# Kernel optimization log

Hardware: AMD Instinct MI355X
Metric: run time of the kernel (lower is better)

Reference implementation:

```python
import jax, jax.numpy as jnp
import numpy as np

N = 131072  # number of attention rows (batch * queries)
M = 100     # number of 2D Gaussian basis functions (10x10 grid in original repo)
TWO_PI = 6.283185307179586


def inv2x2(A):
    """Closed-form inverse and determinant of batched 2x2 matrices."""
    a = A[..., 0, 0]; b = A[..., 0, 1]; c = A[..., 1, 0]; d = A[..., 1, 1]
    det = a * d - b * c
    row0 = jnp.stack([d, -b], axis=-1)
    row1 = jnp.stack([-c, a], axis=-1)
    inv = jnp.stack([row0, row1], axis=-2) / det[..., None, None]
    return inv, det


def setup_inputs() -> dict:
    key = jax.random.key(0)
    k1, k2, k3, k4 = jax.random.split(key, 4)
    # linear canonical parameter eta = Sigma^{-1} mu
    eta = 0.5 * jax.random.normal(k1, (N, 2), dtype=jnp.float32)
    # SPD precision P so that theta[:,2:6] = -0.5 * P (valid exp-family params)
    L = 0.3 * jax.random.normal(k2, (N, 2, 2), dtype=jnp.float32)
    P = L @ jnp.swapaxes(L, -1, -2) + 0.5 * jnp.eye(2, dtype=jnp.float32)
    theta = jnp.concatenate([eta, (-0.5 * P).reshape(N, 4)], axis=1)  # [N,6]
    # Gaussian basis functions: means in [0,1]^2, small diagonal covariances
    basis_mu = jax.random.uniform(k3, (M, 2), dtype=jnp.float32)
    var = jax.random.uniform(k4, (M, 2), dtype=jnp.float32, minval=0.01, maxval=0.05)
    basis_sigma = jax.vmap(jnp.diag)(var)  # [M,2,2]
    return {"theta": theta, "basis_mu": basis_mu, "basis_sigma": basis_sigma}


def reference(theta, basis_mu, basis_sigma):
    # Sigma = symmetrized inverse of (-2 * quadratic canonical params)
    P = -2.0 * theta[:, 2:6].reshape(-1, 2, 2)          # [N,2,2]
    Pinv, _ = inv2x2(P)
    Sigma = 0.5 * (Pinv + jnp.swapaxes(Pinv, -1, -2))   # [N,2,2]
    Mu = jnp.einsum('nij,nj->ni', Sigma, theta[:, 0:2])  # [N,2]
    # r[n,j] = integral N(t; Mu_n, Sigma_n) N(t; mu_j, S_j) dt
    #        = N(Mu_n - mu_j; 0, Sigma_n + S_j)
    C = Sigma[:, None, :, :] + basis_sigma[None, :, :, :]  # [N,M,2,2]
    diff = Mu[:, None, :] - basis_mu[None, :, :]           # [N,M,2]
    Cinv, detC = inv2x2(C)
    quad = jnp.einsum('nmi,nmij,nmj->nm', diff, Cinv, diff)
    r = jnp.exp(-0.5 * quad) / (TWO_PI * jnp.sqrt(detC))   # [N,M]
    return r
```

## Files before the change

kernel.cpp:

```cpp
#include <hip/hip_runtime.h>

#define M_BASIS 100
constexpr float INV_TWO_PI = 0.15915494309189535f;

__global__ __launch_bounds__(256) void cs_kernel(
    const float* __restrict__ theta,
    const float* __restrict__ basis_mu,
    const float* __restrict__ basis_sigma,
    float* __restrict__ out,
    int N)
{
    const int lane = threadIdx.x & 63;
    const int waves_per_block = blockDim.x >> 6;
    const int wave_id = blockIdx.x * waves_per_block + (threadIdx.x >> 6);
    const int num_waves = gridDim.x * waves_per_block;

    const bool active = (lane < (M_BASIS / 2));

    float4 mu2 = make_float4(0.f, 0.f, 0.f, 0.f);
    float4 sA  = make_float4(1.f, 0.f, 0.f, 1.f);
    float4 sB  = make_float4(1.f, 0.f, 0.f, 1.f);
    if (active) {
        mu2 = ((const float4*)basis_mu)[lane];
        sA  = ((const float4*)basis_sigma)[2 * lane];
        sB  = ((const float4*)basis_sigma)[2 * lane + 1];
    }

    #pragma unroll 2
    for (int n = wave_id; n < N; n += num_waves) {
        const float* th = theta + n * 6;
        float2 e  = *(const float2*)(th);
        float2 qa = *(const float2*)(th + 2);
        float2 qb = *(const float2*)(th + 4);

        float detQ = qa.x * qb.y - qa.y * qb.x;
        float r    = __builtin_amdgcn_rcpf(detQ);
        float h    = -0.5f * r;
        float S00  = qb.y * h;
        float S11  = qa.x * h;
        float S01  = (qa.y + qb.x) * (-0.5f * h);
        float Mu0  = S00 * e.x + S01 * e.y;
        float Mu1  = S01 * e.x + S11 * e.y;

        if (active) {
            float c00 = S00 + sA.x, c01 = S01 + sA.y;
            float c10 = S01 + sA.z, c11 = S11 + sA.w;
            float d0 = Mu0 - mu2.x, d1 = Mu1 - mu2.y;
            float detC = c00 * c11 - c01 * c10;
            float rs   = __builtin_amdgcn_rsqf(detC);
            float invC = rs * rs;
            float t = d0 * d0, u = d1 * d1, dd = d0 * d1;
            float num = t * c11 + u * c00 - dd * (c01 + c10);
            float r0 = __expf(-0.5f * num * invC) * (INV_TWO_PI * rs);

            float e00 = S00 + sB.x, e01 = S01 + sB.y;
            float e10 = S01 + sB.z, e11 = S11 + sB.w;
            float f0 = Mu0 - mu2.z, f1 = Mu1 - mu2.w;
            float detE = e00 * e11 - e01 * e10;
            float rsE  = __builtin_amdgcn_rsqf(detE);
            float invE = rsE * rsE;
            float tE = f0 * f0, uE = f1 * f1, ddE = f0 * f1;
            float numE = tE * e11 + uE * e00 - ddE * (e01 + e10);
            float r1 = __expf(-0.5f * numE * invE) * (INV_TWO_PI * rsE);

            ((float2*)(out + (size_t)n * M_BASIS))[lane] = make_float2(r0, r1);
        }
    }
}

extern "C" void kernel_launch(void* const* d_in, const int* in_sizes, int n_in,
                              void* d_out, int out_size, void* d_ws, size_t ws_size,
                              hipStream_t stream) {
    const float* theta      = (const float*)d_in[0];
    const float* basis_mu   = (const float*)d_in[1];
    const float* basis_sig  = (const float*)d_in[2];
    float* out = (float*)d_out;

    int N = in_sizes[0] / 6;
    int block = 256;
    int grid = 4096;
    hipLaunchKernelGGL(cs_kernel, dim3(grid), dim3(block), 0, stream,
                       theta, basis_mu, basis_sig, out, N);
}
```

Measured before the change: 88.30 us.

## Stage output rows in shared memory and write contiguous float4 block stores

Each block now handles a fixed group of 32 rows: every wave computes 8 rows into a shared-memory tile, and after a barrier the whole block writes the tile to global memory with contiguous float4 stores. The grid switches from a grid-stride loop to one block per 32 rows. This targets the partially active waves (only 50 of 64 lanes store 8-byte values) in the output-bandwidth-bound store path. In exchange it adds LDS traffic, a __syncthreads, and far more blocks to launch.

```diff
diff --git a/kernel.cpp b/kernel.cpp
--- a/kernel.cpp
+++ b/kernel.cpp
@@ -1,6 +1,8 @@
 #include <hip/hip_runtime.h>
 
 #define M_BASIS 100
+#define ROWS_PER_BLOCK 32
+#define ROWS_PER_WAVE 8
 constexpr float INV_TWO_PI = 0.15915494309189535f;
 
 __global__ __launch_bounds__(256) void cs_kernel(
@@ -10,11 +12,11 @@
     float* __restrict__ out,
     int N)
 {
-    const int lane = threadIdx.x & 63;
-    const int waves_per_block = blockDim.x >> 6;
-    const int wave_id = blockIdx.x * waves_per_block + (threadIdx.x >> 6);
-    const int num_waves = gridDim.x * waves_per_block;
+    __shared__ float tile[ROWS_PER_BLOCK * M_BASIS];
 
+    const int tid  = threadIdx.x;
+    const int lane = tid & 63;
+    const int wave = tid >> 6;
     const bool active = (lane < (M_BASIS / 2));
 
     float4 mu2 = make_float4(0.f, 0.f, 0.f, 0.f);
@@ -26,45 +28,59 @@
         sB  = ((const float4*)basis_sigma)[2 * lane + 1];
     }
 
-    #pragma unroll 2
-    for (int n = wave_id; n < N; n += num_waves) {
-        const float* th = theta + n * 6;
-        float2 e  = *(const float2*)(th);
-        float2 qa = *(const float2*)(th + 2);
-        float2 qb = *(const float2*)(th + 4);
+    const int row0 = blockIdx.x * ROWS_PER_BLOCK + wave * ROWS_PER_WAVE;
 
-        float detQ = qa.x * qb.y - qa.y * qb.x;
-        float r    = __builtin_amdgcn_rcpf(detQ);
-        float h    = -0.5f * r;
-        float S00  = qb.y * h;
-        float S11  = qa.x * h;
-        float S01  = (qa.y + qb.x) * (-0.5f * h);
-        float Mu0  = S00 * e.x + S01 * e.y;
-        float Mu1  = S01 * e.x + S11 * e.y;
+    #pragma unroll
+    for (int k = 0; k < ROWS_PER_WAVE; ++k) {
+        const int n = row0 + k;
+        if (n < N) {
+            const float* th = theta + n * 6;
+            float2 e  = *(const float2*)(th);
+            float2 qa = *(const float2*)(th + 2);
+            float2 qb = *(const float2*)(th + 4);
 
-        if (active) {
-            float c00 = S00 + sA.x, c01 = S01 + sA.y;
-            float c10 = S01 + sA.z, c11 = S11 + sA.w;
-            float d0 = Mu0 - mu2.x, d1 = Mu1 - mu2.y;
-            float detC = c00 * c11 - c01 * c10;
-            float rs   = __builtin_amdgcn_rsqf(detC);
-            float invC = rs * rs;
-            float t = d0 * d0, u = d1 * d1, dd = d0 * d1;
-            float num = t * c11 + u * c00 - dd * (c01 + c10);
-            float r0 = __expf(-0.5f * num * invC) * (INV_TWO_PI * rs);
+            float detQ = qa.x * qb.y - qa.y * qb.x;
+            float r    = __builtin_amdgcn_rcpf(detQ);
+            float h    = -0.5f * r;
+            float S00  = qb.y * h;
+            float S11  = qa.x * h;
+            float S01  = (qa.y + qb.x) * (-0.5f * h);
+            float Mu0  = S00 * e.x + S01 * e.y;
+            float Mu1  = S01 * e.x + S11 * e.y;
 
-            float e00 = S00 + sB.x, e01 = S01 + sB.y;
-            float e10 = S01 + sB.z, e11 = S11 + sB.w;
-            float f0 = Mu0 - mu2.z, f1 = Mu1 - mu2.w;
-            float detE = e00 * e11 - e01 * e10;
-            float rsE  = __builtin_amdgcn_rsqf(detE);
-            float invE = rsE * rsE;
-            float tE = f0 * f0, uE = f1 * f1, ddE = f0 * f1;
-            float numE = tE * e11 + uE * e00 - ddE * (e01 + e10);
-            float r1 = __expf(-0.5f * numE * invE) * (INV_TWO_PI * rsE);
+            if (active) {
+                float c00 = S00 + sA.x, c01 = S01 + sA.y;
+                float c10 = S01 + sA.z, c11 = S11 + sA.w;
+                float d0 = Mu0 - mu2.x, d1 = Mu1 - mu2.y;
+                float detC = c00 * c11 - c01 * c10;
+                float rs   = __builtin_amdgcn_rsqf(detC);
+                float invC = rs * rs;
+                float num = d0 * d0 * c11 + d1 * d1 * c00 - d0 * d1 * (c01 + c10);
+                float r0 = __expf(-0.5f * num * invC) * (INV_TWO_PI * rs);
 
-            ((float2*)(out + (size_t)n * M_BASIS))[lane] = make_float2(r0, r1);
+                float e00 = S00 + sB.x, e01 = S01 + sB.y;
+                float e10 = S01 + sB.z, e11 = S11 + sB.w;
+                float f0 = Mu0 - mu2.z, f1 = Mu1 - mu2.w;
+                float detE = e00 * e11 - e01 * e10;
+                float rsE  = __builtin_amdgcn_rsqf(detE);
+                float invE = rsE * rsE;
+                float numE = f0 * f0 * e11 + f1 * f1 * e00 - f0 * f1 * (e01 + e10);
+                float r1 = __expf(-0.5f * numE * invE) * (INV_TWO_PI * rsE);
+
+                ((float2*)(tile + (wave * ROWS_PER_WAVE + k) * M_BASIS))[lane] =
+                    make_float2(r0, r1);
+            }
         }
+    }
+
+    __syncthreads();
+
+    const int rows_valid = min(ROWS_PER_BLOCK, N - blockIdx.x * ROWS_PER_BLOCK);
+    const int valid4 = rows_valid * (M_BASIS / 4);
+    float4* obase = (float4*)(out + (size_t)blockIdx.x * ROWS_PER_BLOCK * M_BASIS);
+    const float4* t4 = (const float4*)tile;
+    for (int k = tid; k < valid4; k += 256) {
+        obase[k] = t4[k];
     }
 }
 
@@ -78,7 +94,7 @@
 
     int N = in_sizes[0] / 6;
     int block = 256;
-    int grid = 4096;
+    int grid = (N + ROWS_PER_BLOCK - 1) / ROWS_PER_BLOCK;
     hipLaunchKernelGGL(cs_kernel, dim3(grid), dim3(block), 0, stream,
                        theta, basis_mu, basis_sig, out, N);
 }
```

Measured after the change: 88.65 us. Within noise of the previous version (+0.4%).

## Split into per-row precompute kernel and flat one-output-per-thread kernel

Applied to the files above, without the earlier changes.

Moves the per-row 2x2 inversion and mean computation into a separate kernel that writes 8 floats per row to workspace. The main kernel then uses a flat grid with one output element per thread, reading basis parameters from shared memory. The flat layout gives fully coalesced output stores, where the old wave-per-row loop left 14 of 64 lanes idle. The cost is an extra launch, a workspace round trip of about 4 MB, and redundant row loads and integer division by 100 in every thread.

```diff
diff --git a/kernel.cpp b/kernel.cpp
--- a/kernel.cpp
+++ b/kernel.cpp
@@ -3,69 +3,77 @@
 #define M_BASIS 100
 constexpr float INV_TWO_PI = 0.15915494309189535f;
 
+__global__ __launch_bounds__(256) void row_kernel(
+    const float* __restrict__ theta, float* __restrict__ rp, int N)
+{
+    int n = blockIdx.x * 256 + threadIdx.x;
+    if (n >= N) return;
+    const float* th = theta + n * 6;
+    float2 e  = *(const float2*)(th);
+    float2 qa = *(const float2*)(th + 2);
+    float2 qb = *(const float2*)(th + 4);
+
+    float detQ = qa.x * qb.y - qa.y * qb.x;
+    float r    = __builtin_amdgcn_rcpf(detQ);
+    float h    = -0.5f * r;
+    float S00  = qb.y * h;
+    float S11  = qa.x * h;
+    float S01  = (qa.y + qb.x) * (-0.5f * h);
+    float Mu0  = S00 * e.x + S01 * e.y;
+    float Mu1  = S01 * e.x + S11 * e.y;
+
+    float4* o = (float4*)(rp + 8 * (size_t)n);
+    o[0] = make_float4(S00, S01, S11, Mu0);
+    o[1] = make_float4(Mu1, 2.0f * S01, 0.0f, 0.0f);
+}
+
 __global__ __launch_bounds__(256) void cs_kernel(
-    const float* __restrict__ theta,
+    const float* __restrict__ rp,
     const float* __restrict__ basis_mu,
     const float* __restrict__ basis_sigma,
     float* __restrict__ out,
-    int N)
+    int total)
 {
-    const int lane = threadIdx.x & 63;
-    const int waves_per_block = blockDim.x >> 6;
-    const int wave_id = blockIdx.x * waves_per_block + (threadIdx.x >> 6);
-    const int num_waves = gridDim.x * waves_per_block;
+    __shared__ float B00[M_BASIS], B11[M_BASIS], Bs[M_BASIS], Bp[M_BASIS];
+    __shared__ float M0[M_BASIS], M1[M_BASIS];
 
-    const bool active = (lane < (M_BASIS / 2));
+    int t = threadIdx.x;
+    if (t < M_BASIS) {
+        float4 s = ((const float4*)basis_sigma)[t];
+        float2 m = ((const float2*)basis_mu)[t];
+        B00[t] = s.x; B11[t] = s.w;
+        Bs[t]  = s.y + s.z;
+        Bp[t]  = s.y * s.z;
+        M0[t]  = m.x; M1[t]  = m.y;
+    }
+    __syncthreads();
 
-    float4 mu2 = make_float4(0.f, 0.f, 0.f, 0.f);
-    float4 sA  = make_float4(1.f, 0.f, 0.f, 1.f);
-    float4 sB  = make_float4(1.f, 0.f, 0.f, 1.f);
-    if (active) {
-        mu2 = ((const float4*)basis_mu)[lane];
-        sA  = ((const float4*)basis_sigma)[2 * lane];
-        sB  = ((const float4*)basis_sigma)[2 * lane + 1];
-    }
+    int i = blockIdx.x * 256 + t;
+    if (i >= total) return;
+    unsigned n = (unsigned)i / 100u;
+    unsigned j = (unsigned)i - n * 100u;
 
-    #pragma unroll 2
-    for (int n = wave_id; n < N; n += num_waves) {
-        const float* th = theta + n * 6;
-        float2 e  = *(const float2*)(th);
-        float2 qa = *(const float2*)(th + 2);
-        float2 qb = *(const float2*)(th + 4);
+    const float4* r4 = (const float4*)(rp + 8 * (size_t)n);
+    float4 ra = r4[0];
+    float4 rb = r4[1];
+    float S00 = ra.x, S01 = ra.y, S11 = ra.z, Mu0 = ra.w;
+    float Mu1 = rb.x, twoS01 = rb.y;
 
-        float detQ = qa.x * qb.y - qa.y * qb.x;
-        float r    = __builtin_amdgcn_rcpf(detQ);
-        float h    = -0.5f * r;
-        float S00  = qb.y * h;
-        float S11  = qa.x * h;
-        float S01  = (qa.y + qb.x) * (-0.5f * h);
-        float Mu0  = S00 * e.x + S01 * e.y;
-        float Mu1  = S01 * e.x + S11 * e.y;
+    float c00 = S00 + B00[j];
+    float c11 = S11 + B11[j];
+    float tq  = fmaf(S01, Bs[j], fmaf(S01, S01, Bp[j]));
+    float detC = fmaf(c00, c11, -tq);
 
-        if (active) {
-            float c00 = S00 + sA.x, c01 = S01 + sA.y;
-            float c10 = S01 + sA.z, c11 = S11 + sA.w;
-            float d0 = Mu0 - mu2.x, d1 = Mu1 - mu2.y;
-            float detC = c00 * c11 - c01 * c10;
-            float rs   = __builtin_amdgcn_rsqf(detC);
-            float invC = rs * rs;
-            float t = d0 * d0, u = d1 * d1, dd = d0 * d1;
-            float num = t * c11 + u * c00 - dd * (c01 + c10);
-            float r0 = __expf(-0.5f * num * invC) * (INV_TWO_PI * rs);
+    float d0 = Mu0 - M0[j];
+    float d1 = Mu1 - M1[j];
+    float cs = twoS01 + Bs[j];
+    float num = d0 * d0 * c11;
+    num = fmaf(d1 * d1, c00, num);
+    num = fmaf(-(d0 * d1), cs, num);
 
-            float e00 = S00 + sB.x, e01 = S01 + sB.y;
-            float e10 = S01 + sB.z, e11 = S11 + sB.w;
-            float f0 = Mu0 - mu2.z, f1 = Mu1 - mu2.w;
-            float detE = e00 * e11 - e01 * e10;
-            float rsE  = __builtin_amdgcn_rsqf(detE);
-            float invE = rsE * rsE;
-            float tE = f0 * f0, uE = f1 * f1, ddE = f0 * f1;
-            float numE = tE * e11 + uE * e00 - ddE * (e01 + e10);
-            float r1 = __expf(-0.5f * numE * invE) * (INV_TWO_PI * rsE);
-
-            ((float2*)(out + (size_t)n * M_BASIS))[lane] = make_float2(r0, r1);
-        }
-    }
+    float rs = __builtin_amdgcn_rsqf(detC);
+    float ex = __expf(-0.5f * num * (rs * rs));
+    out[i] = ex * (INV_TWO_PI * rs);
 }
 
 extern "C" void kernel_launch(void* const* d_in, const int* in_sizes, int n_in,
@@ -75,10 +83,16 @@
     const float* basis_mu   = (const float*)d_in[1];
     const float* basis_sig  = (const float*)d_in[2];
     float* out = (float*)d_out;
+    float* rp  = (float*)d_ws;
 
     int N = in_sizes[0] / 6;
-    int block = 256;
-    int grid = 4096;
-    hipLaunchKernelGGL(cs_kernel, dim3(grid), dim3(block), 0, stream,
-                       theta, basis_mu, basis_sig, out, N);
+    int total = out_size;
+
+    int gridA = (N + 255) / 256;
+    hipLaunchKernelGGL(row_kernel, dim3(gridA), dim3(256), 0, stream,
+                       theta, rp, N);
+
+    int gridB = (total + 255) / 256;
+    hipLaunchKernelGGL(cs_kernel, dim3(gridB), dim3(256), 0, stream,
+                       rp, basis_mu, basis_sig, out, total);
 }
```

Result: slower. 103.9 us (+17.7%).

## Process two rows per wave with float4 nontemporal stores of four basis outputs

Applied to the files above, without the earlier changes.

Each wave now handles a pair of rows. Lanes 0-24 compute the first row and lanes 25-49 the second, with four basis functions per lane written as one 16-byte nontemporal store. Basis parameters are pre-reduced into sums and products so fewer ops are needed per element, and the grid is halved to match. The goal is wider, contiguous output stores and more work per wave. The cost is more registers per lane, and the loop drops the last row when N is odd.

```diff
diff --git a/kernel.cpp b/kernel.cpp
--- a/kernel.cpp
+++ b/kernel.cpp
@@ -2,6 +2,8 @@
 
 #define M_BASIS 100
 constexpr float INV_TWO_PI = 0.15915494309189535f;
+
+typedef float vf4 __attribute__((ext_vector_type(4)));
 
 __global__ __launch_bounds__(256) void cs_kernel(
     const float* __restrict__ theta,
@@ -15,19 +17,27 @@
     const int wave_id = blockIdx.x * waves_per_block + (threadIdx.x >> 6);
     const int num_waves = gridDim.x * waves_per_block;
 
-    const bool active = (lane < (M_BASIS / 2));
+    const bool active = (lane < 50);
+    const int sub = (lane < 25) ? lane : lane - 25;
+    const int rsel = (lane < 25) ? 0 : 1;
 
-    float4 mu2 = make_float4(0.f, 0.f, 0.f, 0.f);
-    float4 sA  = make_float4(1.f, 0.f, 0.f, 1.f);
-    float4 sB  = make_float4(1.f, 0.f, 0.f, 1.f);
-    if (active) {
-        mu2 = ((const float4*)basis_mu)[lane];
-        sA  = ((const float4*)basis_sigma)[2 * lane];
-        sB  = ((const float4*)basis_sigma)[2 * lane + 1];
+    float B00[4], B11[4], Bs[4], Bp[4], Mx[4], My[4];
+    #pragma unroll
+    for (int k = 0; k < 4; ++k) {
+        int j = active ? (4 * sub + k) : 0;
+        float4 s = ((const float4*)basis_sigma)[j];
+        float2 m = ((const float2*)basis_mu)[j];
+        B00[k] = s.x; B11[k] = s.w;
+        Bs[k]  = s.y + s.z;
+        Bp[k]  = s.y * s.z;
+        Mx[k]  = m.x; My[k]  = m.y;
     }
 
+    const int pairs = N >> 1;
+
     #pragma unroll 2
-    for (int n = wave_id; n < N; n += num_waves) {
+    for (int p = wave_id; p < pairs; p += num_waves) {
+        const int n = 2 * p + rsel;
         const float* th = theta + n * 6;
         float2 e  = *(const float2*)(th);
         float2 qa = *(const float2*)(th + 2);
@@ -41,29 +51,27 @@
         float S01  = (qa.y + qb.x) * (-0.5f * h);
         float Mu0  = S00 * e.x + S01 * e.y;
         float Mu1  = S01 * e.x + S11 * e.y;
+        float twoS01 = S01 + S01;
 
         if (active) {
-            float c00 = S00 + sA.x, c01 = S01 + sA.y;
-            float c10 = S01 + sA.z, c11 = S11 + sA.w;
-            float d0 = Mu0 - mu2.x, d1 = Mu1 - mu2.y;
-            float detC = c00 * c11 - c01 * c10;
-            float rs   = __builtin_amdgcn_rsqf(detC);
-            float invC = rs * rs;
-            float t = d0 * d0, u = d1 * d1, dd = d0 * d1;
-            float num = t * c11 + u * c00 - dd * (c01 + c10);
-            float r0 = __expf(-0.5f * num * invC) * (INV_TWO_PI * rs);
-
-            float e00 = S00 + sB.x, e01 = S01 + sB.y;
-            float e10 = S01 + sB.z, e11 = S11 + sB.w;
-            float f0 = Mu0 - mu2.z, f1 = Mu1 - mu2.w;
-            float detE = e00 * e11 - e01 * e10;
-            float rsE  = __builtin_amdgcn_rsqf(detE);
-            float invE = rsE * rsE;
-            float tE = f0 * f0, uE = f1 * f1, ddE = f0 * f1;
-            float numE = tE * e11 + uE * e00 - ddE * (e01 + e10);
-            float r1 = __expf(-0.5f * numE * invE) * (INV_TWO_PI * rsE);
-
-            ((float2*)(out + (size_t)n * M_BASIS))[lane] = make_float2(r0, r1);
+            vf4 res;
+            #pragma unroll
+            for (int k = 0; k < 4; ++k) {
+                float c00 = S00 + B00[k];
+                float c11 = S11 + B11[k];
+                float tq  = fmaf(S01, Bs[k], fmaf(S01, S01, Bp[k]));
+                float detC = fmaf(c00, c11, -tq);
+                float d0 = Mu0 - Mx[k];
+                float d1 = Mu1 - My[k];
+                float cs = twoS01 + Bs[k];
+                float num = d0 * d0 * c11;
+                num = fmaf(d1 * d1, c00, num);
+                num = fmaf(-(d0 * d1), cs, num);
+                float rs = __builtin_amdgcn_rsqf(detC);
+                res[k] = __expf(-0.5f * num * (rs * rs)) * (INV_TWO_PI * rs);
+            }
+            vf4* obase = (vf4*)(out + (size_t)p * 2 * M_BASIS);
+            __builtin_nontemporal_store(res, obase + lane);
         }
     }
 }
@@ -78,7 +86,7 @@
 
     int N = in_sizes[0] / 6;
     int block = 256;
-    int grid = 4096;
+    int grid = 2048;
     hipLaunchKernelGGL(cs_kernel, dim3(grid), dim3(block), 0, stream,
                        theta, basis_mu, basis_sig, out, N);
 }
```

Measured after the change: 87.43 us. No clear change (-1.0%).
